# Kernel optimization log

Measured on AMD Instinct MI355X. Metric: run time of the kernel, lower is better.

The kernel has to match this reference:

```python
import jax, jax.numpy as jnp
import numpy as np

B, HP, WP, C = 64, 16, 32, 512   # batch, rows, cols, cnn_feature_size
H = 512                          # hidden_size
L = 2                            # num_layers
MAXH = 32


def setup_inputs() -> dict:
    key = jax.random.key(0)
    ks = jax.random.split(key, 11)
    s = 0.05  # keep gates out of saturation
    return {
        "features":   jax.random.normal(ks[0], (B, HP, WP, C), jnp.float32),
        "pos_emb_fw": jax.random.normal(ks[1], (MAXH + 1, L * 2 * H), jnp.float32) * s,
        "pos_emb_bw": jax.random.normal(ks[2], (MAXH + 1, L * 2 * H), jnp.float32) * s,
        "Wi_fw": jax.random.normal(ks[3], (L, C, 4 * H), jnp.float32) * s,
        "Wh_fw": jax.random.normal(ks[4], (L, H, 4 * H), jnp.float32) * s,
        "bi_fw": jax.random.normal(ks[5], (L, 4 * H), jnp.float32) * s,
        "bh_fw": jax.random.normal(ks[6], (L, 4 * H), jnp.float32) * s,
        "Wi_bw": jax.random.normal(ks[7], (L, C, 4 * H), jnp.float32) * s,
        "Wh_bw": jax.random.normal(ks[8], (L, H, 4 * H), jnp.float32) * s,
        "bi_bw": jax.random.normal(ks[9], (L, 4 * H), jnp.float32) * s,
        "bh_bw": jax.random.normal(ks[10], (L, 4 * H), jnp.float32) * s,
    }


def _stacked_lstm_scan(xs, h0, c0, Wi, Wh, b):
    """xs: (T, N, C); h0, c0: (L, N, H); returns (T, N, H) top-layer outputs."""
    def step(carry, x_t):
        hs, cs = carry
        inp = x_t
        new_h, new_c = [], []
        for l in range(Wi.shape[0]):
            gates = inp @ Wi[l] + hs[l] @ Wh[l] + b[l]          # (N, 4H)
            i_g, f_g, o_g, g_g = jnp.split(gates, 4, axis=-1)   # gate order as in torch chunk
            c_n = jax.nn.sigmoid(f_g) * cs[l] + jax.nn.sigmoid(i_g) * jnp.tanh(g_g)
            h_n = jax.nn.sigmoid(o_g) * jnp.tanh(c_n)
            new_h.append(h_n); new_c.append(c_n)
            inp = h_n
        return (jnp.stack(new_h), jnp.stack(new_c)), inp
    _, ys = jax.lax.scan(step, (h0, c0), xs)
    return ys


def _init_state(pos_emb, row_idx, n, l, h):
    # pos_emb[row_idx]: (N, L*2*H) laid out as [h_1, c_1, ..., h_L, c_L]
    e = pos_emb[row_idx].reshape(n, l, 2, h)
    return e[:, :, 0].transpose(1, 0, 2), e[:, :, 1].transpose(1, 0, 2)  # (L, N, H) each


def reference(features, pos_emb_fw, pos_emb_bw,
              Wi_fw, Wh_fw, bi_fw, bh_fw,
              Wi_bw, Wh_bw, bi_bw, bh_bw):
    b, hp, wp, c = features.shape
    l, _, h4 = Wi_fw.shape
    h = h4 // 4
    n = b * hp  # rows are independent -> fuse into one scan batch

    # (B, Hp, Wp, C) -> (Wp, B*Hp, C), time-major
    xs = features.transpose(2, 0, 1, 3).reshape(wp, n, c)
    # row index i+1 per flattened (b, row) element
    row_idx = jnp.tile(jnp.arange(1, hp + 1), b)  # (N,)

    h0f, c0f = _init_state(pos_emb_fw, row_idx, n, l, h)
    out_fw = _stacked_lstm_scan(xs, h0f, c0f, Wi_fw, Wh_fw, bi_fw + bh_fw)

    h0b, c0b = _init_state(pos_emb_bw, row_idx, n, l, h)
    out_bw = jnp.flip(
        _stacked_lstm_scan(jnp.flip(xs, 0), h0b, c0b, Wi_bw, Wh_bw, bi_bw + bh_bw), 0)

    ctx = jnp.concatenate([out_fw, out_bw], axis=-1)        # (Wp, N, 2H)
    ctx = ctx.reshape(wp, b, hp, 2 * h).transpose(1, 2, 0, 3)  # (B, Hp, Wp, 2H)
    return ctx.reshape(b, hp * wp, 2 * h)
```

## Files before the change

### kernel.cpp

```cpp
#include <hip/hip_runtime.h>
#include <hip/hip_bf16.h>
#include <stdint.h>

#define B_    64
#define HP_   16
#define WP_   32
#define CH_   512
#define HS_   512
#define NSEQ  1024
#define G4    2048
#define KTOT  1024

typedef __hip_bfloat16 bf16_t;
typedef __bf16 bf16x8 __attribute__((ext_vector_type(8)));
typedef float  f32x4  __attribute__((ext_vector_type(4)));

#define WT_OFF   0
#define XBF_OFF  16777216
#define HBUF_OFF 50331648
#define CBUF_OFF 58720256
#define PB_OFF   67108864
#define HB_ELEMS (2*2*1024*512)

__device__ __forceinline__ float sigf(float x) {
    return 1.0f / (1.0f + __expf(-x));
}
__device__ __forceinline__ float tanhfast(float x) {
    x = fminf(fmaxf(x, -15.0f), 15.0f);
    float e = __expf(-2.0f * x);
    return (1.0f - e) / (1.0f + e);
}

__device__ __forceinline__ void gload16(const bf16_t* g, bf16_t* l) {
    __builtin_amdgcn_global_load_lds(
        (const __attribute__((address_space(1))) void*)g,
        (__attribute__((address_space(3))) void*)l, 16, 0, 0);
}

__global__ void k_prep_w(const float* __restrict__ Wi_fw, const float* __restrict__ Wh_fw,
                         const float* __restrict__ Wi_bw, const float* __restrict__ Wh_bw,
                         bf16_t* __restrict__ Wt) {
    int bxi = blockIdx.x;
    int cb = bxi & 63;
    int kb = (bxi >> 6) & 31;
    int u  = bxi >> 11;
    int l  = u >> 1, dir = u & 1;
    const float* Wi = dir ? Wi_bw : Wi_fw;
    const float* Wh = dir ? Wh_bw : Wh_fw;
    int k0 = kb * 32;
    const float* src = (k0 < 512) ? (Wi + (size_t)l*512*2048 + (size_t)k0*2048)
                                  : (Wh + (size_t)l*512*2048 + (size_t)(k0-512)*2048);
    int jblk = cb >> 2, g = cb & 3;
    int sc0 = g*512 + jblk*32;
    int cp0 = cb * 32;
    __shared__ float ld[32][33];
    int tx = threadIdx.x & 31, ty = threadIdx.x >> 5;
#pragma unroll
    for (int i = 0; i < 4; ++i) {
        int kr = ty + i*8;
        ld[kr][tx] = src[(size_t)kr*2048 + sc0 + tx];
    }
    __syncthreads();
#pragma unroll
    for (int i = 0; i < 4; ++i) {
        int cl = ty + i*8;
        Wt[((size_t)u*G4 + cp0 + cl)*KTOT + k0 + tx] = __float2bfloat16(ld[tx][cl]);
    }
}

__global__ void k_prep_bias(const float* __restrict__ bi_fw, const float* __restrict__ bh_fw,
                            const float* __restrict__ bi_bw, const float* __restrict__ bh_bw,
                            float* __restrict__ pb) {
    int id = blockIdx.x * 256 + threadIdx.x;
    if (id >= 4*G4) return;
    int u = id >> 11, cp = id & 2047;
    int l = u >> 1, dir = u & 1;
    int jblk = cp >> 7, rr = cp & 127, g = rr >> 5, jin = rr & 31;
    int col = g*512 + jblk*32 + jin;
    const float* bi = dir ? bi_bw : bi_fw;
    const float* bh = dir ? bh_bw : bh_fw;
    pb[id] = bi[l*G4 + col] + bh[l*G4 + col];
}

__global__ void k_convert_x(const float* __restrict__ f, bf16_t* __restrict__ xbf) {
    int id = blockIdx.x * 256 + threadIdx.x;
    int c8 = id & 63;
    int t  = (id >> 6) & 31;
    int n  = id >> 11;
    const float* s = f + ((size_t)n*WP_ + t)*CH_ + c8*8;
    bf16_t* d = xbf + ((size_t)t*NSEQ + n)*CH_ + c8*8;
#pragma unroll
    for (int i = 0; i < 8; ++i) d[i] = __float2bfloat16(s[i]);
}

__global__ void k_init_state(const float* __restrict__ pe_fw, const float* __restrict__ pe_bw,
                             bf16_t* __restrict__ hbuf, float* __restrict__ cbuf) {
    int id = blockIdx.x * 256 + threadIdx.x;
    int j = id & 511;
    int n = (id >> 9) & 1023;
    int l = (id >> 19) & 1;
    int dir = id >> 20;
    const float* pe = dir ? pe_bw : pe_fw;
    int rowi = (n & 15) + 1;
    float h = pe[(size_t)rowi*2048 + l*1024 + j];
    float c = pe[(size_t)rowi*2048 + l*1024 + 512 + j];
    int pp = (l == 0) ? 1 : 0;
    hbuf[(size_t)pp*HB_ELEMS + (((size_t)dir*2 + l)*NSEQ + n)*HS_ + j] = __float2bfloat16(h);
    cbuf[(((size_t)dir*2 + l)*NSEQ + n)*HS_ + j] = c;
}

__global__ __launch_bounds__(256, 2) void k_phase(
    int p,
    const bf16_t* __restrict__ xbf,
    const bf16_t* __restrict__ Wt,
    const float*  __restrict__ pb,
    bf16_t* __restrict__ hbuf,
    float*  __restrict__ cbuf,
    float*  __restrict__ out) {

    int bx = blockIdx.x;
    int u = bx >> 7;
    int layer = u >> 1;
    int dir = u & 1;
    if (layer == 0 && p >= WP_) return;
    if (layer == 1 && p < 1)    return;

    int bid = bx & 127;
    int rb = bid >> 4;
    int cb = bid & 15;
    int row0 = rb * 128;
    int c0 = cb * 128;

    const bf16_t* hread = hbuf + (size_t)((p + 1) & 1) * HB_ELEMS;
    bf16_t* hwrite      = hbuf + (size_t)(p & 1) * HB_ELEMS;

    const bf16_t* A1;
    const bf16_t* A2;
    int t_out = 0;
    if (layer == 0) {
        int t = dir ? (WP_ - 1 - p) : p;
        A1 = xbf + (size_t)t * NSEQ * CH_;
        A2 = hread + ((size_t)dir*2 + 0) * NSEQ * HS_;
    } else {
        A1 = hread + ((size_t)dir*2 + 0) * NSEQ * HS_;
        A2 = hread + ((size_t)dir*2 + 1) * NSEQ * HS_;
        t_out = dir ? (WP_ - p) : (p - 1);
    }
    const bf16_t* Wu = Wt + (size_t)u * G4 * KTOT;

    __shared__ __align__(16) bf16_t a_lds[128*64];
    __shared__ __align__(16) bf16_t b_lds[128*64];

    int tid = threadIdx.x;
    int lane = tid & 63;
    int wv = tid >> 6;

    f32x4 acc[2][8];
#pragma unroll
    for (int m = 0; m < 2; ++m)
#pragma unroll
        for (int n = 0; n < 8; ++n)
            acc[m][n] = (f32x4){0.f, 0.f, 0.f, 0.f};

    for (int kt = 0; kt < 16; ++kt) {
        const bf16_t* Asrc;
        int kloc;
        if (kt < 8) { Asrc = A1; kloc = kt * 64; }
        else        { Asrc = A2; kloc = kt * 64 - 512; }
#pragma unroll
        for (int q = 0; q < 4; ++q) {
            int id = q*256 + tid;
            int r = id >> 3;
            int s = id & 7;
            int kk = ((s ^ (r & 7)) << 3);
            gload16(Asrc + (size_t)(row0 + r)*512 + kloc + kk,
                    a_lds + (size_t)(q*256 + (wv << 6)) * 8);
        }
#pragma unroll
        for (int q = 0; q < 4; ++q) {
            int id = q*256 + tid;
            int r = id >> 3;
            int s = id & 7;
            int kk = ((s ^ (r & 7)) << 3);
            gload16(Wu + (size_t)(c0 + r)*KTOT + kt*64 + kk,
                    b_lds + (size_t)(q*256 + (wv << 6)) * 8);
        }
        __syncthreads();

        const char* ac = (const char*)a_lds;
        const char* bc = (const char*)b_lds;
#pragma unroll
        for (int ks = 0; ks < 2; ++ks) {
            int kb = (ks << 5) + ((lane >> 4) << 3);
            bf16x8 av[2], bv[8];
#pragma unroll
            for (int m = 0; m < 2; ++m) {
                int row = (wv << 5) + (m << 4) + (lane & 15);
                int byte = row*128 + kb*2;
                byte ^= (row & 7) << 4;
                av[m] = *(const bf16x8*)(ac + byte);
            }
#pragma unroll
            for (int n = 0; n < 8; ++n) {
                int colr = (n << 4) + (lane & 15);
                int byte = colr*128 + kb*2;
                byte ^= (colr & 7) << 4;
                bv[n] = *(const bf16x8*)(bc + byte);
            }
#pragma unroll
            for (int m = 0; m < 2; ++m)
#pragma unroll
                for (int n = 0; n < 8; ++n)
                    acc[m][n] = __builtin_amdgcn_mfma_f32_16x16x32_bf16(av[m], bv[n], acc[m][n], 0, 0, 0);
        }
        __syncthreads();
    }

    float bias[4][2];
#pragma unroll
    for (int g = 0; g < 4; ++g)
#pragma unroll
        for (int jq = 0; jq < 2; ++jq)
            bias[g][jq] = pb[u*G4 + c0 + g*32 + jq*16 + (lane & 15)];

    float* cptr = cbuf + ((size_t)dir*2 + layer) * NSEQ * HS_;
    bf16_t* hw  = hwrite + ((size_t)dir*2 + layer) * NSEQ * HS_;

#pragma unroll
    for (int m = 0; m < 2; ++m) {
#pragma unroll
        for (int jq = 0; jq < 2; ++jq) {
            f32x4 iv = acc[m][0 + jq];
            f32x4 fv = acc[m][2 + jq];
            f32x4 ov = acc[m][4 + jq];
            f32x4 gv = acc[m][6 + jq];
            int j = cb*32 + jq*16 + (lane & 15);
#pragma unroll
            for (int r = 0; r < 4; ++r) {
                int row = (wv << 5) + (m << 4) + ((lane >> 4) << 2) + r;
                int n = row0 + row;
                float ig = sigf(iv[r] + bias[0][jq]);
                float fg = sigf(fv[r] + bias[1][jq]);
                float og = sigf(ov[r] + bias[2][jq]);
                float gg = tanhfast(gv[r] + bias[3][jq]);
                size_t sidx = (size_t)n * HS_ + j;
                float cp = cptr[sidx];
                float cn = fg * cp + ig * gg;
                float hn = og * tanhfast(cn);
                cptr[sidx] = cn;
                hw[sidx] = __float2bfloat16(hn);
                if (layer == 1)
                    out[((size_t)n * WP_ + t_out) * (2*HS_) + (size_t)dir*HS_ + j] = hn;
            }
        }
    }
}

extern "C" void kernel_launch(void* const* d_in, const int* in_sizes, int n_in,
                              void* d_out, int out_size, void* d_ws, size_t ws_size,
                              hipStream_t stream) {
    const float* features = (const float*)d_in[0];
    const float* pe_fw = (const float*)d_in[1];
    const float* pe_bw = (const float*)d_in[2];
    const float* Wi_fw = (const float*)d_in[3];
    const float* Wh_fw = (const float*)d_in[4];
    const float* bi_fw = (const float*)d_in[5];
    const float* bh_fw = (const float*)d_in[6];
    const float* Wi_bw = (const float*)d_in[7];
    const float* Wh_bw = (const float*)d_in[8];
    const float* bi_bw = (const float*)d_in[9];
    const float* bh_bw = (const float*)d_in[10];

    char* ws = (char*)d_ws;
    bf16_t* Wt   = (bf16_t*)(ws + WT_OFF);
    bf16_t* xbf  = (bf16_t*)(ws + XBF_OFF);
    bf16_t* hbuf = (bf16_t*)(ws + HBUF_OFF);
    float*  cbuf = (float*)(ws + CBUF_OFF);
    float*  pb   = (float*)(ws + PB_OFF);
    float*  out  = (float*)d_out;

    k_prep_w<<<dim3(8192), dim3(256), 0, stream>>>(Wi_fw, Wh_fw, Wi_bw, Wh_bw, Wt);
    k_prep_bias<<<dim3(32), dim3(256), 0, stream>>>(bi_fw, bh_fw, bi_bw, bh_bw, pb);
    k_convert_x<<<dim3(8192), dim3(256), 0, stream>>>(features, xbf);
    k_init_state<<<dim3(8192), dim3(256), 0, stream>>>(pe_fw, pe_bw, hbuf, cbuf);

    for (int p = 0; p <= WP_; ++p)
        k_phase<<<dim3(512), dim3(256), 0, stream>>>(p, xbf, Wt, pb, hbuf, cbuf, out);
}
```

Before: 1.144 ms.

## Double-buffer LDS tiles and remap blocks for XCD-local weight reuse

The K loop now uses two LDS buffers, so loading the next 64-wide K slice overlaps with the MFMA work on the current one, and one barrier per iteration is removed. The block index is also remapped so that blocks sharing a column block (and thus weight rows) land on the same XCD, which is meant to improve L2 reuse of weights. The cost is double the LDS footprint (64KB per block), which may limit residency to the declared 2 blocks per CU or fewer.

```diff
diff --git a/kernel.cpp b/kernel.cpp
--- a/kernel.cpp
+++ b/kernel.cpp
@@ -119,15 +119,17 @@
     float*  __restrict__ out) {
 
     int bx = blockIdx.x;
-    int u = bx >> 7;
-    int layer = u >> 1;
-    int dir = u & 1;
+    int xcd   = bx & 7;
+    int layer = (bx >> 8) & 1;
+    int r5    = (bx >> 3) & 31;
+    int dir   = r5 & 1;
+    int cb    = xcd * 2 + ((r5 >> 1) & 1);
+    int rb    = r5 >> 2;
+    int u     = layer * 2 + dir;
+
     if (layer == 0 && p >= WP_) return;
     if (layer == 1 && p < 1)    return;
 
-    int bid = bx & 127;
-    int rb = bid >> 4;
-    int cb = bid & 15;
     int row0 = rb * 128;
     int c0 = cb * 128;
 
@@ -148,8 +150,8 @@
     }
     const bf16_t* Wu = Wt + (size_t)u * G4 * KTOT;
 
-    __shared__ __align__(16) bf16_t a_lds[128*64];
-    __shared__ __align__(16) bf16_t b_lds[128*64];
+    __shared__ __align__(16) bf16_t a_lds[2][128*64];
+    __shared__ __align__(16) bf16_t b_lds[2][128*64];
 
     int tid = threadIdx.x;
     int lane = tid & 63;
@@ -162,7 +164,7 @@
         for (int n = 0; n < 8; ++n)
             acc[m][n] = (f32x4){0.f, 0.f, 0.f, 0.f};
 
-    for (int kt = 0; kt < 16; ++kt) {
+    auto STAGE = [&](int kt, int bufi) {
         const bf16_t* Asrc;
         int kloc;
         if (kt < 8) { Asrc = A1; kloc = kt * 64; }
@@ -174,7 +176,7 @@
             int s = id & 7;
             int kk = ((s ^ (r & 7)) << 3);
             gload16(Asrc + (size_t)(row0 + r)*512 + kloc + kk,
-                    a_lds + (size_t)(q*256 + (wv << 6)) * 8);
+                    a_lds[bufi] + (size_t)(q*256 + (wv << 6)) * 8);
         }
 #pragma unroll
         for (int q = 0; q < 4; ++q) {
@@ -183,12 +185,13 @@
             int s = id & 7;
             int kk = ((s ^ (r & 7)) << 3);
             gload16(Wu + (size_t)(c0 + r)*KTOT + kt*64 + kk,
-                    b_lds + (size_t)(q*256 + (wv << 6)) * 8);
+                    b_lds[bufi] + (size_t)(q*256 + (wv << 6)) * 8);
         }
-        __syncthreads();
-
-        const char* ac = (const char*)a_lds;
-        const char* bc = (const char*)b_lds;
+    };
+
+    auto COMPUTE = [&](int bufi) {
+        const char* ac = (const char*)a_lds[bufi];
+        const char* bc = (const char*)b_lds[bufi];
 #pragma unroll
         for (int ks = 0; ks < 2; ++ks) {
             int kb = (ks << 5) + ((lane >> 4) << 3);
@@ -213,8 +216,18 @@
                 for (int n = 0; n < 8; ++n)
                     acc[m][n] = __builtin_amdgcn_mfma_f32_16x16x32_bf16(av[m], bv[n], acc[m][n], 0, 0, 0);
         }
+    };
+
+    STAGE(0, 0);
+    __syncthreads();
+    int cur = 0;
+    for (int kt = 0; kt < 15; ++kt) {
+        STAGE(kt + 1, cur ^ 1);
+        COMPUTE(cur);
         __syncthreads();
-    }
+        cur ^= 1;
+    }
+    COMPUTE(cur);
 
     float bias[4][2];
 #pragma unroll
```

Result: slower. 1.201 ms (+5.0%).
